# Performance work log

Measured on AMD Instinct MI355X. Metric: run time of the kernel, lower is better.

Reference implementation:

```python
import jax, jax.numpy as jnp
import numpy as np

B, T, D = 8, 2048, 512


def setup_inputs() -> dict:
    key = jax.random.key(0)
    k1, _ = jax.random.split(key)
    h = jax.random.normal(k1, (B, T, D), dtype=jnp.float32)
    k = jnp.ones((), dtype=jnp.float32)  # scalar learned decay param, init='ones'
    return {"h": h, "k": k}


def reference(h, k):
    # h: [B, T, D], k: scalar
    Tn = h.shape[1]
    h_cum = jnp.cumsum(h, axis=1)                                   # [B,T,D]
    h_prev = jnp.pad(h[:, :-1, :], ((0, 0), (1, 0), (0, 0)))        # shift right by 1
    delta = h_cum - h_prev
    delta_mag = jnp.linalg.norm(delta, axis=-1)                      # [B,T]
    t = jnp.arange(Tn)[:, None]
    j = jnp.arange(Tn)[None, :]
    dist = jnp.abs(t - j).astype(jnp.float32)
    decay = jnp.exp(-jax.nn.softplus(k) * dist) * (j <= t)           # [T,T] causal decay
    # importance_{b,i,j} = delta_mag_{b,i} * decay_{i,j}; factor delta_mag out of einsum
    context = jnp.einsum('ij,bjd->bid', decay, h)                    # [B,T,D]
    return jnp.abs(delta_mag[..., None] * context)
```

## Files before the change

kernel.cpp:

```cpp
#include <hip/hip_runtime.h>
#include <math.h>

#define BB 8
#define TT 2048
#define DD 512
#define LL 16
#define CC (TT / LL)
#define D4 (DD / 4)
#define SCT 64
#define NSC (TT / SCT)
#define CPS (SCT / LL)

typedef float floatx4 __attribute__((ext_vector_type(4)));

__device__ __forceinline__ float get_s(const float* kp) {
    float k = *kp;
    return (k > 20.0f) ? k : log1pf(expf(k));
}

__global__ __launch_bounds__(4 * D4) void kA_stats(
    const float* __restrict__ h, const float* __restrict__ kp,
    float* __restrict__ csum, float* __restrict__ cend,
    float* __restrict__ ssum, float* __restrict__ send)
{
    const int blk = blockIdx.x;
    const int b = blk / NSC, sc = blk % NSC;
    const int tid = threadIdx.x;
    const int jj  = tid >> 7;
    const int col = tid & (D4 - 1);
    const float s   = get_s(kp);
    const float a   = expf(-s);
    const float a16 = expf(-s * (float)LL);

    const float4* hp = reinterpret_cast<const float4*>(h)
                     + (size_t)(b * TT + sc * SCT + jj * LL) * D4 + col;

    float sx = 0.f, sy = 0.f, sz = 0.f, sw = 0.f;
    float ex = 0.f, ey = 0.f, ez = 0.f, ew = 0.f;
    #pragma unroll
    for (int i = 0; i < LL; i++) {
        float4 x = hp[(size_t)i * D4];
        sx += x.x; sy += x.y; sz += x.z; sw += x.w;
        ex = fmaf(a, ex, x.x);
        ey = fmaf(a, ey, x.y);
        ez = fmaf(a, ez, x.z);
        ew = fmaf(a, ew, x.w);
    }
    {
        const size_t ci = (size_t)(b * CC + sc * CPS + jj) * D4 + col;
        reinterpret_cast<float4*>(csum)[ci] = make_float4(sx, sy, sz, sw);
        reinterpret_cast<float4*>(cend)[ci] = make_float4(ex, ey, ez, ew);
    }

    __shared__ float4 lsum[CPS][D4];
    __shared__ float4 lend[CPS][D4];
    lsum[jj][col] = make_float4(sx, sy, sz, sw);
    lend[jj][col] = make_float4(ex, ey, ez, ew);
    __syncthreads();

    if (jj == 0) {
        float Sx = 0.f, Sy = 0.f, Sz = 0.f, Sw = 0.f;
        float Ex = 0.f, Ey = 0.f, Ez = 0.f, Ew = 0.f;
        #pragma unroll
        for (int q = 0; q < CPS; q++) {
            float4 sv = lsum[q][col];
            float4 ev = lend[q][col];
            Sx += sv.x; Sy += sv.y; Sz += sv.z; Sw += sv.w;
            Ex = fmaf(a16, Ex, ev.x);
            Ey = fmaf(a16, Ey, ev.y);
            Ez = fmaf(a16, Ez, ev.z);
            Ew = fmaf(a16, Ew, ev.w);
        }
        const size_t si = (size_t)(b * NSC + sc) * D4 + col;
        reinterpret_cast<float4*>(ssum)[si] = make_float4(Sx, Sy, Sz, Sw);
        reinterpret_cast<float4*>(send)[si] = make_float4(Ex, Ey, Ez, Ew);
    }
}

__global__ __launch_bounds__(D4, 4) void kB_out(
    const float* __restrict__ h, const float* __restrict__ kp,
    const float* __restrict__ csum, const float* __restrict__ cend,
    const float* __restrict__ ssum, const float* __restrict__ send,
    float* __restrict__ out)
{
    const int blk = blockIdx.x;
    const int b = blk / CC, c = blk % CC;
    const int sc = c / CPS, j = c & (CPS - 1);
    const int tid = threadIdx.x;
    const int wave = tid >> 6, lane = tid & 63;
    const float s   = get_s(kp);
    const float a   = expf(-s);
    const float a16 = expf(-s * (float)LL);
    const float aSC = expf(-s * (float)SCT);

    const int t0 = c * LL;
    const float4* hp = reinterpret_cast<const float4*>(h)
                     + (size_t)(b * TT + t0) * D4 + tid;

    __shared__ float part[2][LL];

    float4 hv[LL];
    #pragma unroll
    for (int i = 0; i < LL; i++) hv[i] = hp[(size_t)i * D4];

    float px = 0.f, py = 0.f, pz = 0.f, pw = 0.f;
    if (t0 > 0) {
        float4 pv = *(hp - (ptrdiff_t)D4);
        px = pv.x; py = pv.y; pz = pv.z; pw = pv.w;
    }

    float cox = 0.f, coy = 0.f, coz = 0.f, cow = 0.f;
    float ccx = 0.f, ccy = 0.f, ccz = 0.f, ccw = 0.f;
    if (sc > 0) {
        const float4* ss4 = reinterpret_cast<const float4*>(ssum)
                          + (size_t)(b * NSC) * D4 + tid;
        const float4* se4 = reinterpret_cast<const float4*>(send)
                          + (size_t)(b * NSC) * D4 + tid;
        float w = 1.f;
        #pragma unroll
        for (int d = 0; d < NSC - 1; d++) {
            const int   q    = (d < sc) ? (sc - 1 - d) : 0;
            const float live = (d < sc) ? 1.f : 0.f;
            float4 sv = ss4[(size_t)q * D4];
            float4 ev = se4[(size_t)q * D4];
            cox = fmaf(live, sv.x, cox);
            coy = fmaf(live, sv.y, coy);
            coz = fmaf(live, sv.z, coz);
            cow = fmaf(live, sv.w, cow);
            const float wl = w * live;
            ccx = fmaf(wl, ev.x, ccx);
            ccy = fmaf(wl, ev.y, ccy);
            ccz = fmaf(wl, ev.z, ccz);
            ccw = fmaf(wl, ev.w, ccw);
            w *= aSC;
        }
    }
    if (j > 0) {
        const float4* cs4 = reinterpret_cast<const float4*>(csum)
                          + (size_t)(b * CC + sc * CPS) * D4 + tid;
        const float4* ce4 = reinterpret_cast<const float4*>(cend)
                          + (size_t)(b * CC + sc * CPS) * D4 + tid;
        float cIx = 0.f, cIy = 0.f, cIz = 0.f, cIw = 0.f;
        float w = 1.f;
        #pragma unroll
        for (int d = 0; d < CPS - 1; d++) {
            const int   q    = (d < j) ? (j - 1 - d) : 0;
            const float live = (d < j) ? 1.f : 0.f;
            float4 sv = cs4[(size_t)q * D4];
            float4 ev = ce4[(size_t)q * D4];
            cox = fmaf(live, sv.x, cox);
            coy = fmaf(live, sv.y, coy);
            coz = fmaf(live, sv.z, coz);
            cow = fmaf(live, sv.w, cow);
            const float wl = w * live;
            cIx = fmaf(wl, ev.x, cIx);
            cIy = fmaf(wl, ev.y, cIy);
            cIz = fmaf(wl, ev.z, cIz);
            cIw = fmaf(wl, ev.w, cIw);
            w *= a16;
        }
        const float a32 = a16 * a16;
        const float wj  = (j == 1) ? a16 : (j == 2) ? a32 : a32 * a16;
        ccx = fmaf(wj, ccx, cIx);
        ccy = fmaf(wj, ccy, cIy);
        ccz = fmaf(wj, ccz, cIz);
        ccw = fmaf(wj, ccw, cIw);
    }

    float r[LL];
    #pragma unroll
    for (int i = 0; i < LL; i++) {
        float4 x = hv[i];
        cox += x.x; coy += x.y; coz += x.z; cow += x.w;
        float dx = cox - px, dy = coy - py, dz = coz - pz, dw = cow - pw;
        r[i] = dx * dx + dy * dy + dz * dz + dw * dw;
        px = x.x; py = x.y; pz = x.z; pw = x.w;
    }

    #pragma unroll
    for (int m = 1; m < 64; m <<= 1) {
        #pragma unroll
        for (int i = 0; i < LL; i++) r[i] += __shfl_xor(r[i], m, 64);
    }
    if (lane == 0) {
        #pragma unroll
        for (int i = 0; i < LL; i++) part[wave][i] = r[i];
    }
    __syncthreads();

    float mag[LL];
    #pragma unroll
    for (int i = 0; i < LL; i++) mag[i] = sqrtf(part[0][i] + part[1][i]);

    floatx4* op = reinterpret_cast<floatx4*>(out)
                + (size_t)(b * TT + t0) * D4 + tid;
    #pragma unroll
    for (int i = 0; i < LL; i++) {
        float4 x = hv[i];
        ccx = fmaf(a, ccx, x.x);
        ccy = fmaf(a, ccy, x.y);
        ccz = fmaf(a, ccz, x.z);
        ccw = fmaf(a, ccw, x.w);
        float m = mag[i];
        floatx4 o;
        o.x = fabsf(m * ccx); o.y = fabsf(m * ccy);
        o.z = fabsf(m * ccz); o.w = fabsf(m * ccw);
        __builtin_nontemporal_store(o, op + (size_t)i * D4);
    }
}

extern "C" void kernel_launch(void* const* d_in, const int* in_sizes, int n_in,
                              void* d_out, int out_size, void* d_ws, size_t ws_size,
                              hipStream_t stream) {
    const float* h  = (const float*)d_in[0];
    const float* kp = (const float*)d_in[1];
    float* out = (float*)d_out;

    const size_t NC  = (size_t)BB * CC * DD;
    const size_t NSb = (size_t)BB * NSC * DD;
    float* csum = (float*)d_ws;
    float* cend = csum + NC;
    float* ssum = cend + NC;
    float* send = ssum + NSb;

    kA_stats<<<dim3(BB * NSC), dim3(4 * D4), 0, stream>>>(h, kp, csum, cend, ssum, send);
    kB_out  <<<dim3(BB * CC),  dim3(D4),     0, stream>>>(h, kp, csum, cend, ssum, send, out);
}
```

Measured before the change: 101.2 us.

## Recompute chunk stats in shared memory inside output kernel, drop csum/cend buffers

The output kernel now processes a whole 64-step superchunk per block (512 threads, four 16-step chunks). It recomputes per-chunk sums and decayed ends in shared memory instead of reading csum/cend written by the stats kernel. This removes the global write and read of the per-chunk intermediates and their workspace. In exchange there are 4x fewer, larger blocks (256 blocks), an extra block barrier, and higher register pressure under launch bounds of 512 threads with min 2 blocks per CU.

After: 93.66 us. 1.08x faster.

```diff
diff --git a/kernel.cpp b/kernel.cpp
--- a/kernel.cpp
+++ b/kernel.cpp
@@ -20,7 +20,6 @@
 
 __global__ __launch_bounds__(4 * D4) void kA_stats(
     const float* __restrict__ h, const float* __restrict__ kp,
-    float* __restrict__ csum, float* __restrict__ cend,
     float* __restrict__ ssum, float* __restrict__ send)
 {
     const int blk = blockIdx.x;
@@ -45,11 +44,6 @@
         ey = fmaf(a, ey, x.y);
         ez = fmaf(a, ez, x.z);
         ew = fmaf(a, ew, x.w);
-    }
-    {
-        const size_t ci = (size_t)(b * CC + sc * CPS + jj) * D4 + col;
-        reinterpret_cast<float4*>(csum)[ci] = make_float4(sx, sy, sz, sw);
-        reinterpret_cast<float4*>(cend)[ci] = make_float4(ex, ey, ez, ew);
     }
 
     __shared__ float4 lsum[CPS][D4];
@@ -77,31 +71,46 @@
     }
 }
 
-__global__ __launch_bounds__(D4, 4) void kB_out(
+__global__ __launch_bounds__(4 * D4, 2) void kB_out(
     const float* __restrict__ h, const float* __restrict__ kp,
-    const float* __restrict__ csum, const float* __restrict__ cend,
     const float* __restrict__ ssum, const float* __restrict__ send,
     float* __restrict__ out)
 {
     const int blk = blockIdx.x;
-    const int b = blk / CC, c = blk % CC;
-    const int sc = c / CPS, j = c & (CPS - 1);
+    const int b = blk / NSC, sc = blk % NSC;
     const int tid = threadIdx.x;
-    const int wave = tid >> 6, lane = tid & 63;
+    const int jj  = tid >> 7;
+    const int col = tid & (D4 - 1);
+    const int gw   = (tid >> 6) & 1;
+    const int lane = tid & 63;
     const float s   = get_s(kp);
     const float a   = expf(-s);
     const float a16 = expf(-s * (float)LL);
     const float aSC = expf(-s * (float)SCT);
 
-    const int t0 = c * LL;
+    const int t0 = sc * SCT + jj * LL;
     const float4* hp = reinterpret_cast<const float4*>(h)
-                     + (size_t)(b * TT + t0) * D4 + tid;
-
-    __shared__ float part[2][LL];
+                     + (size_t)(b * TT + t0) * D4 + col;
+
+    __shared__ float4 lsum[CPS][D4];
+    __shared__ float4 lend[CPS][D4];
+    __shared__ float part[CPS][2][LL];
 
     float4 hv[LL];
-    #pragma unroll
-    for (int i = 0; i < LL; i++) hv[i] = hp[(size_t)i * D4];
+    float sx = 0.f, sy = 0.f, sz = 0.f, sw = 0.f;
+    float ex = 0.f, ey = 0.f, ez = 0.f, ew = 0.f;
+    #pragma unroll
+    for (int i = 0; i < LL; i++) {
+        float4 x = hp[(size_t)i * D4];
+        hv[i] = x;
+        sx += x.x; sy += x.y; sz += x.z; sw += x.w;
+        ex = fmaf(a, ex, x.x);
+        ey = fmaf(a, ey, x.y);
+        ez = fmaf(a, ez, x.z);
+        ew = fmaf(a, ew, x.w);
+    }
+    lsum[jj][col] = make_float4(sx, sy, sz, sw);
+    lend[jj][col] = make_float4(ex, ey, ez, ew);
 
     float px = 0.f, py = 0.f, pz = 0.f, pw = 0.f;
     if (t0 > 0) {
@@ -113,9 +122,9 @@
     float ccx = 0.f, ccy = 0.f, ccz = 0.f, ccw = 0.f;
     if (sc > 0) {
         const float4* ss4 = reinterpret_cast<const float4*>(ssum)
-                          + (size_t)(b * NSC) * D4 + tid;
+                          + (size_t)(b * NSC) * D4 + col;
         const float4* se4 = reinterpret_cast<const float4*>(send)
-                          + (size_t)(b * NSC) * D4 + tid;
+                          + (size_t)(b * NSC) * D4 + col;
         float w = 1.f;
         #pragma unroll
         for (int d = 0; d < NSC - 1; d++) {
@@ -135,19 +144,18 @@
             w *= aSC;
         }
     }
-    if (j > 0) {
-        const float4* cs4 = reinterpret_cast<const float4*>(csum)
-                          + (size_t)(b * CC + sc * CPS) * D4 + tid;
-        const float4* ce4 = reinterpret_cast<const float4*>(cend)
-                          + (size_t)(b * CC + sc * CPS) * D4 + tid;
+
+    __syncthreads();
+
+    if (jj > 0) {
         float cIx = 0.f, cIy = 0.f, cIz = 0.f, cIw = 0.f;
         float w = 1.f;
         #pragma unroll
         for (int d = 0; d < CPS - 1; d++) {
-            const int   q    = (d < j) ? (j - 1 - d) : 0;
-            const float live = (d < j) ? 1.f : 0.f;
-            float4 sv = cs4[(size_t)q * D4];
-            float4 ev = ce4[(size_t)q * D4];
+            const int   q    = (d < jj) ? (jj - 1 - d) : 0;
+            const float live = (d < jj) ? 1.f : 0.f;
+            float4 sv = lsum[q][col];
+            float4 ev = lend[q][col];
             cox = fmaf(live, sv.x, cox);
             coy = fmaf(live, sv.y, coy);
             coz = fmaf(live, sv.z, coz);
@@ -160,7 +168,7 @@
             w *= a16;
         }
         const float a32 = a16 * a16;
-        const float wj  = (j == 1) ? a16 : (j == 2) ? a32 : a32 * a16;
+        const float wj  = (jj == 1) ? a16 : (jj == 2) ? a32 : a32 * a16;
         ccx = fmaf(wj, ccx, cIx);
         ccy = fmaf(wj, ccy, cIy);
         ccz = fmaf(wj, ccz, cIz);
@@ -184,16 +192,16 @@
     }
     if (lane == 0) {
         #pragma unroll
-        for (int i = 0; i < LL; i++) part[wave][i] = r[i];
+        for (int i = 0; i < LL; i++) part[jj][gw][i] = r[i];
     }
     __syncthreads();
 
     float mag[LL];
     #pragma unroll
-    for (int i = 0; i < LL; i++) mag[i] = sqrtf(part[0][i] + part[1][i]);
+    for (int i = 0; i < LL; i++) mag[i] = sqrtf(part[jj][0][i] + part[jj][1][i]);
 
     floatx4* op = reinterpret_cast<floatx4*>(out)
-                + (size_t)(b * TT + t0) * D4 + tid;
+                + (size_t)(b * TT + t0) * D4 + col;
     #pragma unroll
     for (int i = 0; i < LL; i++) {
         float4 x = hv[i];
@@ -216,13 +224,10 @@
     const float* kp = (const float*)d_in[1];
     float* out = (float*)d_out;
 
-    const size_t NC  = (size_t)BB * CC * DD;
     const size_t NSb = (size_t)BB * NSC * DD;
-    float* csum = (float*)d_ws;
-    float* cend = csum + NC;
-    float* ssum = cend + NC;
+    float* ssum = (float*)d_ws;
     float* send = ssum + NSb;
 
-    kA_stats<<<dim3(BB * NSC), dim3(4 * D4), 0, stream>>>(h, kp, csum, cend, ssum, send);
-    kB_out  <<<dim3(BB * CC),  dim3(D4),     0, stream>>>(h, kp, csum, cend, ssum, send, out);
-}
+    kA_stats<<<dim3(BB * NSC), dim3(4 * D4), 0, stream>>>(h, kp, ssum, send);
+    kB_out  <<<dim3(BB * NSC), dim3(4 * D4), 0, stream>>>(h, kp, ssum, send, out);
+}
```

## Replace two-level chunk/superchunk prefix with flat per-chunk serial scan

Applied to the files above, without the earlier changes.

Drops the superchunk summary level and has each output block accumulate over every preceding 16-row chunk directly, in an 8-way unrolled dynamic loop. The stats kernel becomes one block per chunk with no shared-memory reduction, and the occupancy hint for the output kernel is lowered. This removes the extra reduction stage and superchunk buffers. In exchange, per-block prefix work grows linearly with chunk index, so total reads of the chunk summaries grow quadratically.

Measured after the change: 104.8 us. +3.6%, slower.

```diff
diff --git a/kernel.cpp b/kernel.cpp
--- a/kernel.cpp
+++ b/kernel.cpp
@@ -7,9 +7,6 @@
 #define LL 16
 #define CC (TT / LL)
 #define D4 (DD / 4)
-#define SCT 64
-#define NSC (TT / SCT)
-#define CPS (SCT / LL)
 
 typedef float floatx4 __attribute__((ext_vector_type(4)));
 
@@ -18,22 +15,19 @@
     return (k > 20.0f) ? k : log1pf(expf(k));
 }
 
-__global__ __launch_bounds__(4 * D4) void kA_stats(
+
+__global__ __launch_bounds__(D4) void kA_stats(
     const float* __restrict__ h, const float* __restrict__ kp,
-    float* __restrict__ csum, float* __restrict__ cend,
-    float* __restrict__ ssum, float* __restrict__ send)
+    float* __restrict__ csum, float* __restrict__ cend)
 {
     const int blk = blockIdx.x;
-    const int b = blk / NSC, sc = blk % NSC;
+    const int b = blk / CC, c = blk % CC;
     const int tid = threadIdx.x;
-    const int jj  = tid >> 7;
-    const int col = tid & (D4 - 1);
-    const float s   = get_s(kp);
-    const float a   = expf(-s);
-    const float a16 = expf(-s * (float)LL);
+    const float s = get_s(kp);
+    const float a = expf(-s);
 
     const float4* hp = reinterpret_cast<const float4*>(h)
-                     + (size_t)(b * TT + sc * SCT + jj * LL) * D4 + col;
+                     + (size_t)(b * TT + c * LL) * D4 + tid;
 
     float sx = 0.f, sy = 0.f, sz = 0.f, sw = 0.f;
     float ex = 0.f, ey = 0.f, ez = 0.f, ew = 0.f;
@@ -46,52 +40,23 @@
         ez = fmaf(a, ez, x.z);
         ew = fmaf(a, ew, x.w);
     }
-    {
-        const size_t ci = (size_t)(b * CC + sc * CPS + jj) * D4 + col;
-        reinterpret_cast<float4*>(csum)[ci] = make_float4(sx, sy, sz, sw);
-        reinterpret_cast<float4*>(cend)[ci] = make_float4(ex, ey, ez, ew);
-    }
-
-    __shared__ float4 lsum[CPS][D4];
-    __shared__ float4 lend[CPS][D4];
-    lsum[jj][col] = make_float4(sx, sy, sz, sw);
-    lend[jj][col] = make_float4(ex, ey, ez, ew);
-    __syncthreads();
-
-    if (jj == 0) {
-        float Sx = 0.f, Sy = 0.f, Sz = 0.f, Sw = 0.f;
-        float Ex = 0.f, Ey = 0.f, Ez = 0.f, Ew = 0.f;
-        #pragma unroll
-        for (int q = 0; q < CPS; q++) {
-            float4 sv = lsum[q][col];
-            float4 ev = lend[q][col];
-            Sx += sv.x; Sy += sv.y; Sz += sv.z; Sw += sv.w;
-            Ex = fmaf(a16, Ex, ev.x);
-            Ey = fmaf(a16, Ey, ev.y);
-            Ez = fmaf(a16, Ez, ev.z);
-            Ew = fmaf(a16, Ew, ev.w);
-        }
-        const size_t si = (size_t)(b * NSC + sc) * D4 + col;
-        reinterpret_cast<float4*>(ssum)[si] = make_float4(Sx, Sy, Sz, Sw);
-        reinterpret_cast<float4*>(send)[si] = make_float4(Ex, Ey, Ez, Ew);
-    }
+    const size_t ci = (size_t)(b * CC + c) * D4 + tid;
+    reinterpret_cast<float4*>(csum)[ci] = make_float4(sx, sy, sz, sw);
+    reinterpret_cast<float4*>(cend)[ci] = make_float4(ex, ey, ez, ew);
 }
 
-__global__ __launch_bounds__(D4, 4) void kB_out(
+__global__ __launch_bounds__(D4, 2) void kB_out(
     const float* __restrict__ h, const float* __restrict__ kp,
     const float* __restrict__ csum, const float* __restrict__ cend,
-    const float* __restrict__ ssum, const float* __restrict__ send,
     float* __restrict__ out)
 {
     const int blk = blockIdx.x;
     const int b = blk / CC, c = blk % CC;
-    const int sc = c / CPS, j = c & (CPS - 1);
     const int tid = threadIdx.x;
     const int wave = tid >> 6, lane = tid & 63;
     const float s   = get_s(kp);
     const float a   = expf(-s);
     const float a16 = expf(-s * (float)LL);
-    const float aSC = expf(-s * (float)SCT);
 
     const int t0 = c * LL;
     const float4* hp = reinterpret_cast<const float4*>(h)
@@ -111,60 +76,32 @@
 
     float cox = 0.f, coy = 0.f, coz = 0.f, cow = 0.f;
     float ccx = 0.f, ccy = 0.f, ccz = 0.f, ccw = 0.f;
-    if (sc > 0) {
-        const float4* ss4 = reinterpret_cast<const float4*>(ssum)
-                          + (size_t)(b * NSC) * D4 + tid;
-        const float4* se4 = reinterpret_cast<const float4*>(send)
-                          + (size_t)(b * NSC) * D4 + tid;
+    if (c > 0) {
+        const float4* cs4 = reinterpret_cast<const float4*>(csum)
+                          + (size_t)(b * CC) * D4 + tid;
+        const float4* ce4 = reinterpret_cast<const float4*>(cend)
+                          + (size_t)(b * CC) * D4 + tid;
         float w = 1.f;
-        #pragma unroll
-        for (int d = 0; d < NSC - 1; d++) {
-            const int   q    = (d < sc) ? (sc - 1 - d) : 0;
-            const float live = (d < sc) ? 1.f : 0.f;
-            float4 sv = ss4[(size_t)q * D4];
-            float4 ev = se4[(size_t)q * D4];
-            cox = fmaf(live, sv.x, cox);
-            coy = fmaf(live, sv.y, coy);
-            coz = fmaf(live, sv.z, coz);
-            cow = fmaf(live, sv.w, cow);
-            const float wl = w * live;
-            ccx = fmaf(wl, ev.x, ccx);
-            ccy = fmaf(wl, ev.y, ccy);
-            ccz = fmaf(wl, ev.z, ccz);
-            ccw = fmaf(wl, ev.w, ccw);
-            w *= aSC;
+        for (int base = 0; base < c; base += 8) {
+            #pragma unroll
+            for (int u = 0; u < 8; u++) {
+                const int   dd   = base + u;
+                const int   q    = (dd < c) ? (c - 1 - dd) : 0;
+                const float live = (dd < c) ? 1.f : 0.f;
+                float4 sv = cs4[(size_t)q * D4];
+                float4 ev = ce4[(size_t)q * D4];
+                cox = fmaf(live, sv.x, cox);
+                coy = fmaf(live, sv.y, coy);
+                coz = fmaf(live, sv.z, coz);
+                cow = fmaf(live, sv.w, cow);
+                const float wl = w * live;
+                ccx = fmaf(wl, ev.x, ccx);
+                ccy = fmaf(wl, ev.y, ccy);
+                ccz = fmaf(wl, ev.z, ccz);
+                ccw = fmaf(wl, ev.w, ccw);
+                w *= a16;
+            }
         }
-    }
-    if (j > 0) {
-        const float4* cs4 = reinterpret_cast<const float4*>(csum)
-                          + (size_t)(b * CC + sc * CPS) * D4 + tid;
-        const float4* ce4 = reinterpret_cast<const float4*>(cend)
-                          + (size_t)(b * CC + sc * CPS) * D4 + tid;
-        float cIx = 0.f, cIy = 0.f, cIz = 0.f, cIw = 0.f;
-        float w = 1.f;
-        #pragma unroll
-        for (int d = 0; d < CPS - 1; d++) {
-            const int   q    = (d < j) ? (j - 1 - d) : 0;
-            const float live = (d < j) ? 1.f : 0.f;
-            float4 sv = cs4[(size_t)q * D4];
-            float4 ev = ce4[(size_t)q * D4];
-            cox = fmaf(live, sv.x, cox);
-            coy = fmaf(live, sv.y, coy);
-            coz = fmaf(live, sv.z, coz);
-            cow = fmaf(live, sv.w, cow);
-            const float wl = w * live;
-            cIx = fmaf(wl, ev.x, cIx);
-            cIy = fmaf(wl, ev.y, cIy);
-            cIz = fmaf(wl, ev.z, cIz);
-            cIw = fmaf(wl, ev.w, cIw);
-            w *= a16;
-        }
-        const float a32 = a16 * a16;
-        const float wj  = (j == 1) ? a16 : (j == 2) ? a32 : a32 * a16;
-        ccx = fmaf(wj, ccx, cIx);
-        ccy = fmaf(wj, ccy, cIy);
-        ccz = fmaf(wj, ccz, cIz);
-        ccw = fmaf(wj, ccw, cIw);
     }
 
     float r[LL];
@@ -216,13 +153,10 @@
     const float* kp = (const float*)d_in[1];
     float* out = (float*)d_out;
 
-    const size_t NC  = (size_t)BB * CC * DD;
-    const size_t NSb = (size_t)BB * NSC * DD;
+    const size_t NC = (size_t)BB * CC * DD;
     float* csum = (float*)d_ws;
     float* cend = csum + NC;
-    float* ssum = cend + NC;
-    float* send = ssum + NSb;
 
-    kA_stats<<<dim3(BB * NSC), dim3(4 * D4), 0, stream>>>(h, kp, csum, cend, ssum, send);
-    kB_out  <<<dim3(BB * CC),  dim3(D4),     0, stream>>>(h, kp, csum, cend, ssum, send, out);
+    kA_stats<<<dim3(BB * CC), dim3(D4), 0, stream>>>(h, kp, csum, cend);
+    kB_out  <<<dim3(BB * CC), dim3(D4), 0, stream>>>(h, kp, csum, cend, out);
 }
```
